# Kernel optimization log

Hardware: AMD Instinct MI355X
Metric: run time of the kernel (lower is better)

## Reference

```python
import jax, jax.numpy as jnp
import numpy as np
import math

B, T, D, H = 8, 1024, 512, 8
DK = D // H


def setup_inputs() -> dict:
    key = jax.random.key(0)
    ks = jax.random.split(key, 16)
    f = lambda k, s: jax.random.normal(k, s, dtype=jnp.float32)
    p = lambda k, s: jax.random.normal(k, s, dtype=jnp.float32) * 0.02
    return {
        "query": f(ks[0], (B, T, D)),
        "key": f(ks[1], (B, T, D)),
        "value": f(ks[2], (B, T, D)),
        "pos_embedding": f(ks[3], (B, T, D)),
        "Wq": p(ks[4], (D, D)), "bq": p(ks[5], (D,)),
        "Wk": p(ks[6], (D, D)), "bk": p(ks[7], (D,)),
        "Wv": p(ks[8], (D, D)), "bv": p(ks[9], (D,)),
        "Wp": p(ks[10], (D, D)),
        "u_bias": p(ks[11], (H, DK)),
        "v_bias": p(ks[12], (H, DK)),
        "Wo": p(ks[13], (D, D)), "bo": p(ks[14], (D,)),
    }


def _rel_shift(pos_score):
    # pos_score: [B, H, T, T]  -> Transformer-XL relative shift via pad/reshape
    b, h, t1, t2 = pos_score.shape
    padded = jnp.concatenate(
        [jnp.zeros((b, h, t1, 1), pos_score.dtype), pos_score], axis=-1
    )  # [B,H,T,T+1]
    padded = padded.reshape(b, h, t2 + 1, t1)
    return padded[:, :, 1:].reshape(b, h, t1, t2)


def reference(query, key, value, pos_embedding, Wq, bq, Wk, bk, Wv, bv, Wp,
              u_bias, v_bias, Wo, bo):
    q = (query @ Wq + bq).reshape(B, T, H, DK)          # [B,T,H,DK]
    k = (key @ Wk + bk).reshape(B, T, H, DK)
    v = (value @ Wv + bv).reshape(B, T, H, DK)
    p = (pos_embedding @ Wp).reshape(B, T, H, DK)

    content_score = jnp.einsum("bihd,bjhd->bhij", q + u_bias, k)
    pos_score = jnp.einsum("bihd,bjhd->bhij", q + v_bias, p)
    pos_score = _rel_shift(pos_score)

    score = (content_score + pos_score) / math.sqrt(D)  # note: sqrt(d_model)
    attn = jax.nn.softmax(score, axis=-1)               # dropout: eval mode
    context = jnp.einsum("bhij,bjhd->bihd", attn, v).reshape(B, T, D)
    return context @ Wo + bo
```

## Files before the change

### kernel.cpp

```cpp
#include <hip/hip_runtime.h>

#define B_ 8
#define T_ 1024
#define D_ 512
#define H_ 8
#define DK_ 64

typedef __bf16 bf16x8 __attribute__((ext_vector_type(8)));
typedef float f32x4 __attribute__((ext_vector_type(4)));

#define MFMA16(a, b, c) __builtin_amdgcn_mfma_f32_16x16x32_bf16(a, b, c, 0, 0, 0)

__device__ __forceinline__ bf16x8 pack8(float4 a, float4 b) {
  bf16x8 r;
  r[0] = (__bf16)a.x; r[1] = (__bf16)a.y; r[2] = (__bf16)a.z; r[3] = (__bf16)a.w;
  r[4] = (__bf16)b.x; r[5] = (__bf16)b.y; r[6] = (__bf16)b.z; r[7] = (__bf16)b.w;
  return r;
}

__device__ __forceinline__ void load_lds16(const void* g, void* l) {
  __builtin_amdgcn_global_load_lds(
      (const __attribute__((address_space(1))) void*)g,
      (__attribute__((address_space(3))) void*)l, 16, 0, 0);
}

__global__ __launch_bounds__(256) void cvt_x(const float* __restrict__ q,
                                             const float* __restrict__ k,
                                             const float* __restrict__ v,
                                             const float* __restrict__ p,
                                             __bf16* __restrict__ dst) {
  const float* src = (blockIdx.y == 0) ? q
                   : (blockIdx.y == 1) ? k
                   : (blockIdx.y == 2) ? v : p;
  const size_t e = ((size_t)blockIdx.x * 256 + threadIdx.x) * 8;
  const int row = (int)(e >> 9);
  const int kk = (int)(e & 511);
  const int phys = (kk & ~63) | ((((kk >> 3) & 7) ^ (row & 7)) << 3);
  float4 a = *(const float4*)(src + e);
  float4 b = *(const float4*)(src + e + 4);
  *(bf16x8*)(dst + (size_t)blockIdx.y * 4194304 + (size_t)row * 512 + phys) =
      pack8(a, b);
}

__global__ __launch_bounds__(256) void cvt_w(const float* __restrict__ w0,
                                             const float* __restrict__ w1,
                                             const float* __restrict__ w2,
                                             const float* __restrict__ w3,
                                             const float* __restrict__ w4,
                                             __bf16* __restrict__ wt) {
  __shared__ float Ts[64][65];
  const float* W = (blockIdx.z == 0) ? w0
                 : (blockIdx.z == 1) ? w1
                 : (blockIdx.z == 2) ? w2
                 : (blockIdx.z == 3) ? w3 : w4;
  const int tid = threadIdx.x;
  const int kt = blockIdx.x * 64, nt = blockIdx.y * 64;
  const int r = tid >> 2, co = (tid & 3) * 16;
#pragma unroll
  for (int q = 0; q < 4; ++q)
    *(float4*)&Ts[r][co + q * 4] =
        *(const float4*)(W + (size_t)(kt + r) * 512 + nt + co + q * 4);
  __syncthreads();
  bf16x8 o0, o1;
#pragma unroll
  for (int q = 0; q < 8; ++q) o0[q] = (__bf16)Ts[co + q][r];
#pragma unroll
  for (int q = 0; q < 8; ++q) o1[q] = (__bf16)Ts[co + 8 + q][r];
  const int key = r & 7;
  __bf16* dst =
      wt + (size_t)blockIdx.z * 262144 + (size_t)(nt + r) * 512 + kt;
  *(bf16x8*)(dst + (((co >> 3) ^ key) << 3)) = o0;
  *(bf16x8*)(dst + ((((co >> 3) + 1) ^ key) << 3)) = o1;
}

template <int PHASE>
__global__ __launch_bounds__(256, 4) void gemm_dma(
    const __bf16* __restrict__ Xc, const __bf16* __restrict__ ctxA,
    const __bf16* __restrict__ Wt, const float* __restrict__ bq,
    const float* __restrict__ bk, const float* __restrict__ bv,
    const float* __restrict__ bo, const float* __restrict__ u,
    const float* __restrict__ v, __bf16* __restrict__ quB,
    __bf16* __restrict__ qvB, __bf16* __restrict__ kB,
    __bf16* __restrict__ vT, __bf16* __restrict__ pB,
    float* __restrict__ out) {
  __shared__ __bf16 smem[17408];
  __bf16* As = smem;
  __bf16* Bs = smem + 8192;
  const int tid = threadIdx.x;
  const int z = blockIdx.z;
  const int wave = tid >> 6, lane = tid & 63, l16 = lane & 15, quad = lane >> 4;
  const int wm = wave & 1, wn = wave >> 1;
  const int m0 = blockIdx.x * 128, n0 = blockIdx.y * 128;

  const __bf16* Ag = PHASE ? ctxA : Xc + (size_t)z * (8192 * 512);
  const __bf16* Bg = Wt + (size_t)(PHASE ? 4 : z) * (512 * 512);

  const int drow = tid >> 3, dch = (tid & 7) * 8;
  char* ldsA = (char*)As + (tid & 192) * 16;
  char* ldsB = (char*)Bs + (tid & 192) * 16;
  const int keyc = l16 & 7;

  f32x4 acc[4][4];
#pragma unroll
  for (int rb = 0; rb < 4; ++rb)
#pragma unroll
    for (int cb = 0; cb < 4; ++cb) acc[rb][cb] = 0.f;

#pragma unroll 1
  for (int k0 = 0; k0 < 512; k0 += 64) {
    __syncthreads();
#pragma unroll
    for (int c4 = 0; c4 < 4; ++c4) {
      load_lds16(Ag + (size_t)(m0 + c4 * 32 + drow) * 512 + k0 + dch,
                 ldsA + c4 * 4096);
      load_lds16(Bg + (size_t)(n0 + c4 * 32 + drow) * 512 + k0 + dch,
                 ldsB + c4 * 4096);
    }
    __syncthreads();
#pragma unroll
    for (int s = 0; s < 2; ++s) {
      const int ph = ((s * 4 + quad) ^ keyc) << 3;
      bf16x8 afr[4], bfr[4];
#pragma unroll
      for (int rb = 0; rb < 4; ++rb)
        afr[rb] = *(const bf16x8*)&As[(wm * 64 + rb * 16 + l16) * 64 + ph];
#pragma unroll
      for (int cb = 0; cb < 4; ++cb)
        bfr[cb] = *(const bf16x8*)&Bs[(wn * 64 + cb * 16 + l16) * 64 + ph];
#pragma unroll
      for (int rb = 0; rb < 4; ++rb)
#pragma unroll
        for (int cb = 0; cb < 4; ++cb)
          acc[rb][cb] = MFMA16(afr[rb], bfr[cb], acc[rb][cb]);
    }
  }

  if (PHASE == 1) {
#pragma unroll
    for (int rb = 0; rb < 4; ++rb)
#pragma unroll
      for (int cb = 0; cb < 4; ++cb) {
        const int col = n0 + wn * 64 + cb * 16 + l16;
        const float bb = bo[col];
#pragma unroll
        for (int r = 0; r < 4; ++r) {
          const int row = m0 + wm * 64 + rb * 16 + quad * 4 + r;
          out[(size_t)row * 512 + col] = acc[rb][cb][r] + bb;
        }
      }
    return;
  }

  if (z == 2) {
    __syncthreads();
    __bf16* Tt = smem;
#pragma unroll
    for (int rb = 0; rb < 4; ++rb)
#pragma unroll
      for (int cb = 0; cb < 4; ++cb) {
        const int cl = wn * 64 + cb * 16 + l16;
        const float bb = bv[n0 + cl];
#pragma unroll
        for (int r = 0; r < 4; ++r) {
          const int rl = wm * 64 + rb * 16 + quad * 4 + r;
          Tt[cl * 136 + rl] = (__bf16)(acc[rb][cb][r] + bb);
        }
      }
    __syncthreads();
    const int r2 = tid >> 1, ch = (tid & 1) * 64;
    const int hh = (n0 + r2) >> 6, dkk = (n0 + r2) & 63;
    const int bI = m0 >> 10, t0 = m0 & 1023;
    __bf16* dst = vT + (((size_t)(bI * H_ + hh)) * DK_ + dkk) * T_ + t0 + ch;
    const int vkey = dkk & 7;
#pragma unroll
    for (int q = 0; q < 8; ++q)
      *(bf16x8*)(dst + ((q ^ vkey) * 8)) = *(const bf16x8*)&Tt[r2 * 136 + ch + q * 8];
    return;
  }

#pragma unroll
  for (int rb = 0; rb < 4; ++rb)
#pragma unroll
    for (int cb = 0; cb < 4; ++cb) {
      const int col = n0 + wn * 64 + cb * 16 + l16;
      const float bb = (z == 0) ? bq[col] : (z == 1) ? bk[col] : 0.f;
      const float uu = (z == 0) ? u[col] : 0.f;
      const float vv = (z == 0) ? v[col] : 0.f;
#pragma unroll
      for (int r = 0; r < 4; ++r) {
        const int row = m0 + wm * 64 + rb * 16 + quad * 4 + r;
        const float val = acc[rb][cb][r] + bb;
        const int bI = row >> 10, tt = row & 1023;
        const int hh = col >> 6, dk = col & 63;
        const int dks = (z == 0)
            ? dk
            : ((dk & 7) | ((((dk >> 3) ^ tt) & 7) << 3));
        const size_t idx = (((size_t)(bI * H_ + hh)) * T_ + tt) * DK_ + dks;
        if (z == 0) {
          quB[idx] = (__bf16)(val + uu);
          qvB[idx] = (__bf16)(val + vv);
        } else if (z == 1) {
          kB[idx] = (__bf16)val;
        } else {
          pB[idx] = (__bf16)val;
        }
      }
    }
}

__global__ __launch_bounds__(256, 4) void attn_mfma(
    const __bf16* __restrict__ qu, const __bf16* __restrict__ qv,
    const __bf16* __restrict__ kbuf, const __bf16* __restrict__ vT,
    const __bf16* __restrict__ pbuf, __bf16* __restrict__ ctx) {
  constexpr float SCALE = 0.044194173824159216f;
  __shared__ __bf16 smemA[4488];
  __shared__ __bf16 Vt[4096];
  __shared__ __bf16 Pb[8192];
  __bf16* Kt = smemA;
  __bf16* Rs = smemA;
  __bf16* Pa = Pb;

  const int tid = threadIdx.x;
  const int wave = tid >> 6, lane = tid & 63, l16 = lane & 15, quad = lane >> 4;
  const int g = blockIdx.x;
  const int bhq = (g & 7) * 8 + (g >> 7);
  const int i0 = ((g >> 3) & 15) * 64;
  const size_t bh = (size_t)bhq * T_ * DK_;
  const __bf16* QU = qu + bh;
  const __bf16* QV = qv + bh;
  const __bf16* Kg = kbuf + bh;
  const __bf16* Vg = vT + bh;
  const __bf16* Pg = pbuf + bh;

  bf16x8 quA[2], qvw[2], qv4[2];
  {
    const int rw = i0 + wave * 16 + l16;
    const int r4g = i0 + 64 + l16;
    const int r4 = (r4g < T_) ? r4g : T_ - 1;
#pragma unroll
    for (int s = 0; s < 2; ++s) {
      const int ko = s * 32 + quad * 8;
      quA[s] = *(const bf16x8*)&QU[(size_t)rw * DK_ + ko];
      qvw[s] = *(const bf16x8*)&QV[(size_t)rw * DK_ + ko];
      qv4[s] = *(const bf16x8*)&QV[(size_t)r4 * DK_ + ko];
    }
  }

  f32x4 Oacc[4];
#pragma unroll
  for (int cb = 0; cb < 4; ++cb) Oacc[cb] = 0.f;
  float lrun[4];
#pragma unroll
  for (int r = 0; r < 4; ++r) lrun[r] = 0.f;

  const int rbase = wave * 16 + quad * 4;
  const int keyr = l16 & 7;
  const int keyp = (l16 + 7) & 7;
  const int drow = tid >> 3;
  const int dch = (tid & 7) * 8;
  char* ldsK = (char*)Kt + (tid & 192) * 16;
  char* ldsV = (char*)Vt + (tid & 192) * 16;
  char* ldsP = (char*)Pb + (tid & 192) * 16;

#pragma unroll 1
  for (int jt = 0; jt < 16; ++jt) {
    const int j0 = jt * 64;
    int cs = T_ - 65 + j0 - i0;
    if (cs < 0) cs += T_;
    if (cs >= T_) cs -= T_;

    __syncthreads();
    load_lds16(Kg + (size_t)(j0 + drow) * 64 + dch, ldsK);
    load_lds16(Kg + (size_t)(j0 + 32 + drow) * 64 + dch, ldsK + 4096);
    load_lds16(Vg + (size_t)drow * T_ + j0 + dch, ldsV);
    load_lds16(Vg + (size_t)(32 + drow) * T_ + j0 + dch, ldsV + 4096);
#pragma unroll
    for (int c = 0; c < 4; ++c) {
      int prow = cs + c * 32 + drow;
      if (prow >= T_) prow -= T_;
      load_lds16(Pg + (size_t)prow * 64 + dch, ldsP + c * 4096);
    }
    __syncthreads();

    f32x4 sA[4];
#pragma unroll
    for (int cb = 0; cb < 4; ++cb) sA[cb] = 0.f;
#pragma unroll
    for (int s = 0; s < 2; ++s)
#pragma unroll
      for (int cb = 0; cb < 4; ++cb) {
        bf16x8 kf = *(const bf16x8*)&Kt[(cb * 16 + l16) * 64 +
                                        (((s * 4 + quad) ^ keyr) << 3)];
        sA[cb] = MFMA16(quA[s], kf, sA[cb]);
      }

    __syncthreads();

#pragma unroll
    for (int c = 0; c < 5; ++c) {
      const int cb = 3 - wave + c;
      f32x4 rc = 0.f;
#pragma unroll
      for (int s = 0; s < 2; ++s) {
        bf16x8 pf = *(const bf16x8*)&Pb[(cb * 16 + l16) * 64 +
                                        (((s * 4 + quad) ^ keyp) << 3)];
        rc = MFMA16(qvw[s], pf, rc);
      }
      const int col = cb * 16 + l16;
#pragma unroll
      for (int rr = 0; rr < 4; ++rr) {
        const int dj = col + rbase + rr - 64;
        if (dj >= 0 && dj < 64) Rs[(rbase + rr) * 68 + dj] = (__bf16)rc[rr];
      }
    }
    {
      const int cb = wave;
      f32x4 rc = 0.f;
#pragma unroll
      for (int s = 0; s < 2; ++s) {
        bf16x8 pf = *(const bf16x8*)&Pb[(cb * 16 + l16) * 64 +
                                        (((s * 4 + quad) ^ keyp) << 3)];
        rc = MFMA16(qv4[s], pf, rc);
      }
      if (quad == 0) Rs[64 * 68 + cb * 16 + l16] = (__bf16)rc[0];
    }
    __syncthreads();

#pragma unroll
    for (int r = 0; r < 4; ++r) {
#pragma unroll
      for (int cb = 0; cb < 4; ++cb) {
        const int di = rbase + r;
        const int dj = cb * 16 + l16;
        const int ji = (j0 + dj) - (i0 + di);
        float pos = 0.f;
        if (ji != 1) pos = (float)Rs[(di + (ji >= 2 ? 1 : 0)) * 68 + dj];
        const float w_ = __expf((sA[cb][r] + pos) * SCALE);
        lrun[r] += w_;
        Pa[di * 64 + (dj & 7) + ((((dj >> 3) ^ di) & 7) << 3)] = (__bf16)w_;
      }
    }

#pragma unroll
    for (int s = 0; s < 2; ++s) {
      bf16x8 ap = *(const bf16x8*)&Pa[(wave * 16 + l16) * 64 +
                                      (((s * 4 + quad) ^ keyr) << 3)];
#pragma unroll
      for (int cb = 0; cb < 4; ++cb) {
        bf16x8 bv = *(const bf16x8*)&Vt[(cb * 16 + l16) * 64 +
                                        (((s * 4 + quad) ^ keyr) << 3)];
        Oacc[cb] = MFMA16(ap, bv, Oacc[cb]);
      }
    }
  }

  float inv[4];
#pragma unroll
  for (int r = 0; r < 4; ++r) {
    float L = lrun[r];
    L += __shfl_xor(L, 1);
    L += __shfl_xor(L, 2);
    L += __shfl_xor(L, 4);
    L += __shfl_xor(L, 8);
    inv[r] = 1.f / L;
  }
  const int b = bhq >> 3, h = bhq & 7;
#pragma unroll
  for (int cb = 0; cb < 4; ++cb)
#pragma unroll
    for (int r = 0; r < 4; ++r) {
      const int row = i0 + rbase + r;
      const int chunk = cb * 2 + (l16 >> 3);
      const int col = h * DK_ + ((chunk ^ (row & 7)) << 3) + (l16 & 7);
      ctx[((size_t)(b * T_ + row)) * D_ + col] = (__bf16)(Oacc[cb][r] * inv[r]);
    }
}

extern "C" void kernel_launch(void* const* d_in, const int* in_sizes, int n_in,
                              void* d_out, int out_size, void* d_ws,
                              size_t ws_size, hipStream_t stream) {
  const float* query = (const float*)d_in[0];
  const float* key   = (const float*)d_in[1];
  const float* value = (const float*)d_in[2];
  const float* pos   = (const float*)d_in[3];
  const float* Wq = (const float*)d_in[4];
  const float* bq = (const float*)d_in[5];
  const float* Wk = (const float*)d_in[6];
  const float* bk = (const float*)d_in[7];
  const float* Wv = (const float*)d_in[8];
  const float* bv = (const float*)d_in[9];
  const float* Wp = (const float*)d_in[10];
  const float* ub = (const float*)d_in[11];
  const float* vbias = (const float*)d_in[12];
  const float* Wo = (const float*)d_in[13];
  const float* bo = (const float*)d_in[14];
  float* out = (float*)d_out;

  char* ws = (char*)d_ws;
  const size_t ACT = (size_t)8192 * 512 * 2;
  __bf16* Xc  = (__bf16*)ws;
  __bf16* quB = (__bf16*)(ws + 4 * ACT);
  __bf16* qvB = (__bf16*)(ws + 5 * ACT);
  __bf16* kB  = (__bf16*)(ws + 6 * ACT);
  __bf16* pB  = (__bf16*)(ws + 7 * ACT);
  __bf16* vT  = (__bf16*)(ws + 8 * ACT);
  __bf16* Wt  = (__bf16*)(ws + 9 * ACT);
  __bf16* ctx = Xc;

  cvt_x<<<dim3(2048, 4), 256, 0, stream>>>(query, key, value, pos, Xc);
  cvt_w<<<dim3(8, 8, 5), 256, 0, stream>>>(Wq, Wk, Wv, Wp, Wo, Wt);

  gemm_dma<0><<<dim3(64, 4, 4), 256, 0, stream>>>(
      Xc, nullptr, Wt, bq, bk, bv, bo, ub, vbias, quB, qvB, kB, vT, pB,
      nullptr);

  attn_mfma<<<dim3(1024), 256, 0, stream>>>(quB, qvB, kB, vT, pB, ctx);

  gemm_dma<1><<<dim3(64, 4, 1), 256, 0, stream>>>(
      nullptr, ctx, Wt, bq, bk, bv, bo, ub, vbias, quB, qvB, kB, vT, pB,
      out);
}
```

Baseline: 257.5 us.

## Fuse fp32-to-bf16 input conversion into projection GEMM and stage stores via LDS

Drops the separate cvt_x pass: the projection GEMM now reads fp32 activations directly, converts them to bf16 in registers, and writes them swizzled into LDS. This saves writing and re-reading a full bf16 copy of all four inputs. The projection epilogue now goes through an LDS transpose tile so q/k/p outputs are written with 16-byte vector stores instead of scalar scattered stores. The attention loop also replaces the first barrier with a partial vmcnt wait, so the K tile can be consumed while V/P loads are still in flight. The cost is that GEMM A-loads become synchronous register loads instead of direct global-to-LDS DMA.

```diff
diff --git a/kernel.cpp b/kernel.cpp
--- a/kernel.cpp
+++ b/kernel.cpp
@@ -22,24 +22,6 @@
   __builtin_amdgcn_global_load_lds(
       (const __attribute__((address_space(1))) void*)g,
       (__attribute__((address_space(3))) void*)l, 16, 0, 0);
-}
-
-__global__ __launch_bounds__(256) void cvt_x(const float* __restrict__ q,
-                                             const float* __restrict__ k,
-                                             const float* __restrict__ v,
-                                             const float* __restrict__ p,
-                                             __bf16* __restrict__ dst) {
-  const float* src = (blockIdx.y == 0) ? q
-                   : (blockIdx.y == 1) ? k
-                   : (blockIdx.y == 2) ? v : p;
-  const size_t e = ((size_t)blockIdx.x * 256 + threadIdx.x) * 8;
-  const int row = (int)(e >> 9);
-  const int kk = (int)(e & 511);
-  const int phys = (kk & ~63) | ((((kk >> 3) & 7) ^ (row & 7)) << 3);
-  float4 a = *(const float4*)(src + e);
-  float4 b = *(const float4*)(src + e + 4);
-  *(bf16x8*)(dst + (size_t)blockIdx.y * 4194304 + (size_t)row * 512 + phys) =
-      pack8(a, b);
 }
 
 __global__ __launch_bounds__(256) void cvt_w(const float* __restrict__ w0,
@@ -75,14 +57,15 @@
 
 template <int PHASE>
 __global__ __launch_bounds__(256, 4) void gemm_dma(
-    const __bf16* __restrict__ Xc, const __bf16* __restrict__ ctxA,
-    const __bf16* __restrict__ Wt, const float* __restrict__ bq,
-    const float* __restrict__ bk, const float* __restrict__ bv,
-    const float* __restrict__ bo, const float* __restrict__ u,
-    const float* __restrict__ v, __bf16* __restrict__ quB,
-    __bf16* __restrict__ qvB, __bf16* __restrict__ kB,
-    __bf16* __restrict__ vT, __bf16* __restrict__ pB,
-    float* __restrict__ out) {
+    const float* __restrict__ qf, const float* __restrict__ kf,
+    const float* __restrict__ vf, const float* __restrict__ pf,
+    const __bf16* __restrict__ ctxA, const __bf16* __restrict__ Wt,
+    const float* __restrict__ bq, const float* __restrict__ bk,
+    const float* __restrict__ bv, const float* __restrict__ bo,
+    const float* __restrict__ ub, const float* __restrict__ vb,
+    __bf16* __restrict__ quB, __bf16* __restrict__ qvB,
+    __bf16* __restrict__ kB, __bf16* __restrict__ vT,
+    __bf16* __restrict__ pB, float* __restrict__ out) {
   __shared__ __bf16 smem[17408];
   __bf16* As = smem;
   __bf16* Bs = smem + 8192;
@@ -92,7 +75,7 @@
   const int wm = wave & 1, wn = wave >> 1;
   const int m0 = blockIdx.x * 128, n0 = blockIdx.y * 128;
 
-  const __bf16* Ag = PHASE ? ctxA : Xc + (size_t)z * (8192 * 512);
+  const float* Af = (z == 0) ? qf : (z == 1) ? kf : (z == 2) ? vf : pf;
   const __bf16* Bg = Wt + (size_t)(PHASE ? 4 : z) * (512 * 512);
 
   const int drow = tid >> 3, dch = (tid & 7) * 8;
@@ -110,11 +93,24 @@
   for (int k0 = 0; k0 < 512; k0 += 64) {
     __syncthreads();
 #pragma unroll
-    for (int c4 = 0; c4 < 4; ++c4) {
-      load_lds16(Ag + (size_t)(m0 + c4 * 32 + drow) * 512 + k0 + dch,
-                 ldsA + c4 * 4096);
+    for (int c4 = 0; c4 < 4; ++c4)
       load_lds16(Bg + (size_t)(n0 + c4 * 32 + drow) * 512 + k0 + dch,
                  ldsB + c4 * 4096);
+    if (PHASE == 1) {
+#pragma unroll
+      for (int c4 = 0; c4 < 4; ++c4)
+        load_lds16(ctxA + (size_t)(m0 + c4 * 32 + drow) * 512 + k0 + dch,
+                   ldsA + c4 * 4096);
+    } else {
+#pragma unroll
+      for (int c4 = 0; c4 < 4; ++c4) {
+        const int row = c4 * 32 + drow;
+        const float* s = Af + (size_t)(m0 + row) * 512 + k0 + dch;
+        float4 a0 = *(const float4*)s;
+        float4 a1 = *(const float4*)(s + 4);
+        *(bf16x8*)&As[row * 64 + ((((dch >> 3) ^ row) & 7) << 3)] =
+            pack8(a0, a1);
+      }
     }
     __syncthreads();
 #pragma unroll
@@ -151,8 +147,9 @@
     return;
   }
 
+  __syncthreads();
+
   if (z == 2) {
-    __syncthreads();
     __bf16* Tt = smem;
 #pragma unroll
     for (int rb = 0; rb < 4; ++rb)
@@ -174,38 +171,43 @@
     const int vkey = dkk & 7;
 #pragma unroll
     for (int q = 0; q < 8; ++q)
-      *(bf16x8*)(dst + ((q ^ vkey) * 8)) = *(const bf16x8*)&Tt[r2 * 136 + ch + q * 8];
+      *(bf16x8*)(dst + ((q ^ vkey) * 8)) =
+          *(const bf16x8*)&Tt[r2 * 136 + ch + q * 8];
     return;
   }
 
-#pragma unroll
-  for (int rb = 0; rb < 4; ++rb)
-#pragma unroll
-    for (int cb = 0; cb < 4; ++cb) {
-      const int col = n0 + wn * 64 + cb * 16 + l16;
-      const float bb = (z == 0) ? bq[col] : (z == 1) ? bk[col] : 0.f;
-      const float uu = (z == 0) ? u[col] : 0.f;
-      const float vv = (z == 0) ? v[col] : 0.f;
-#pragma unroll
-      for (int r = 0; r < 4; ++r) {
-        const int row = m0 + wm * 64 + rb * 16 + quad * 4 + r;
-        const float val = acc[rb][cb][r] + bb;
-        const int bI = row >> 10, tt = row & 1023;
-        const int hh = col >> 6, dk = col & 63;
-        const int dks = (z == 0)
-            ? dk
-            : ((dk & 7) | ((((dk >> 3) ^ tt) & 7) << 3));
-        const size_t idx = (((size_t)(bI * H_ + hh)) * T_ + tt) * DK_ + dks;
-        if (z == 0) {
-          quB[idx] = (__bf16)(val + uu);
-          qvB[idx] = (__bf16)(val + vv);
-        } else if (z == 1) {
-          kB[idx] = (__bf16)val;
-        } else {
-          pB[idx] = (__bf16)val;
+  __bf16* Tt = smem;
+  const int trow = tid & 127, hs = tid >> 7;
+  const int bI = m0 >> 10, tt = (m0 & 1023) + trow;
+  const int hh = (n0 >> 6) + hs;
+  const size_t obase = (((size_t)(bI * H_ + hh)) * T_ + tt) * DK_;
+  const int npass = (z == 0) ? 2 : 1;
+#pragma unroll 1
+  for (int pass = 0; pass < npass; ++pass) {
+#pragma unroll
+    for (int rb = 0; rb < 4; ++rb)
+#pragma unroll
+      for (int cb = 0; cb < 4; ++cb) {
+        const int cl = wn * 64 + cb * 16 + l16;
+        const int col = n0 + cl;
+        const float b0 = (z == 0) ? bq[col] : (z == 1) ? bk[col] : 0.f;
+        const float b1 = (z == 0) ? (pass ? vb[col] : ub[col]) : 0.f;
+#pragma unroll
+        for (int r = 0; r < 4; ++r) {
+          const int rl = wm * 64 + rb * 16 + quad * 4 + r;
+          Tt[rl * 136 + cl] = (__bf16)((acc[rb][cb][r] + b0) + b1);
         }
       }
-    }
+    __syncthreads();
+    __bf16* dst = ((z == 0) ? (pass ? qvB : quB) : (z == 1) ? kB : pB) + obase;
+#pragma unroll
+    for (int qd = 0; qd < 8; ++qd) {
+      const int c = (z == 0) ? qd : (qd ^ (tt & 7));
+      *(bf16x8*)(dst + c * 8) =
+          *(const bf16x8*)&Tt[trow * 136 + hs * 64 + qd * 8];
+    }
+    if (pass + 1 < npass) __syncthreads();
+  }
 }
 
 __global__ __launch_bounds__(256, 4) void attn_mfma(
@@ -272,6 +274,7 @@
     __syncthreads();
     load_lds16(Kg + (size_t)(j0 + drow) * 64 + dch, ldsK);
     load_lds16(Kg + (size_t)(j0 + 32 + drow) * 64 + dch, ldsK + 4096);
+    __builtin_amdgcn_sched_barrier(0);
     load_lds16(Vg + (size_t)drow * T_ + j0 + dch, ldsV);
     load_lds16(Vg + (size_t)(32 + drow) * T_ + j0 + dch, ldsV + 4096);
 #pragma unroll
@@ -280,7 +283,8 @@
       if (prow >= T_) prow -= T_;
       load_lds16(Pg + (size_t)prow * 64 + dch, ldsP + c * 4096);
     }
-    __syncthreads();
+    asm volatile("s_waitcnt vmcnt(6)" ::: "memory");
+    __builtin_amdgcn_s_barrier();
 
     f32x4 sA[4];
 #pragma unroll
@@ -294,7 +298,8 @@
         sA[cb] = MFMA16(quA[s], kf, sA[cb]);
       }
 
-    __syncthreads();
+    asm volatile("s_waitcnt vmcnt(0)" ::: "memory");
+    __builtin_amdgcn_s_barrier();
 
 #pragma unroll
     for (int c = 0; c < 5; ++c) {
@@ -398,25 +403,23 @@
 
   char* ws = (char*)d_ws;
   const size_t ACT = (size_t)8192 * 512 * 2;
-  __bf16* Xc  = (__bf16*)ws;
-  __bf16* quB = (__bf16*)(ws + 4 * ACT);
-  __bf16* qvB = (__bf16*)(ws + 5 * ACT);
-  __bf16* kB  = (__bf16*)(ws + 6 * ACT);
-  __bf16* pB  = (__bf16*)(ws + 7 * ACT);
-  __bf16* vT  = (__bf16*)(ws + 8 * ACT);
-  __bf16* Wt  = (__bf16*)(ws + 9 * ACT);
-  __bf16* ctx = Xc;
-
-  cvt_x<<<dim3(2048, 4), 256, 0, stream>>>(query, key, value, pos, Xc);
+  __bf16* quB = (__bf16*)ws;
+  __bf16* qvB = (__bf16*)(ws + 1 * ACT);
+  __bf16* kB  = (__bf16*)(ws + 2 * ACT);
+  __bf16* pB  = (__bf16*)(ws + 3 * ACT);
+  __bf16* vT  = (__bf16*)(ws + 4 * ACT);
+  __bf16* ctx = (__bf16*)(ws + 5 * ACT);
+  __bf16* Wt  = (__bf16*)(ws + 6 * ACT);
+
   cvt_w<<<dim3(8, 8, 5), 256, 0, stream>>>(Wq, Wk, Wv, Wp, Wo, Wt);
 
   gemm_dma<0><<<dim3(64, 4, 4), 256, 0, stream>>>(
-      Xc, nullptr, Wt, bq, bk, bv, bo, ub, vbias, quB, qvB, kB, vT, pB,
-      nullptr);
+      query, key, value, pos, nullptr, Wt, bq, bk, bv, bo, ub, vbias,
+      quB, qvB, kB, vT, pB, nullptr);
 
   attn_mfma<<<dim3(1024), 256, 0, stream>>>(quB, qvB, kB, vT, pB, ctx);
 
   gemm_dma<1><<<dim3(64, 4, 1), 256, 0, stream>>>(
-      nullptr, ctx, Wt, bq, bk, bv, bo, ub, vbias, quB, qvB, kB, vT, pB,
-      out);
-}
+      nullptr, nullptr, nullptr, nullptr, ctx, Wt, bq, bk, bv, bo, ub, vbias,
+      quB, qvB, kB, vT, pB, out);
+}
```

New measurement: 247.1 us. 1.04x faster.
